# Optimization experiments

Measured on AMD Instinct MI355X. Metric: run time of the kernel, lower is better.

## Reference

```python
import jax, jax.numpy as jnp
import numpy as np

WINDOW_SIZE = 11
SIGMA = 1.5

def _gauss1d(n, sigma):
    xs = (jnp.arange(n) - n // 2).astype(jnp.float32)
    g = jnp.exp(-(xs ** 2) / (2.0 * sigma ** 2))
    return g / g.sum()

def _blur3d(v, g):
    # Separable 3D Gaussian blur == dense outer-product 3D window used by the
    # original (the torch window is an exact outer product of 1D gaussians).
    C = v.shape[1]
    k = g.shape[0]
    p = k // 2
    for ax in range(3):
        kshape = [1, 1, 1]
        kshape[ax] = k
        w = jnp.broadcast_to(g.reshape(tuple(kshape))[None, None], (C, 1) + tuple(kshape))
        pad = [(0, 0), (0, 0), (0, 0)]
        pad[ax] = (p, p)
        v = jax.lax.conv_general_dilated(
            v, w, window_strides=(1, 1, 1), padding=pad,
            dimension_numbers=('NCDHW', 'OIDHW', 'NCDHW'),
            feature_group_count=C)
    return v

def _ssim(a, b, size_average=True):
    g = _gauss1d(WINDOW_SIZE, SIGMA)
    mu1 = _blur3d(a, g)
    mu2 = _blur3d(b, g)
    mu1_sq = mu1 * mu1
    mu2_sq = mu2 * mu2
    sigma1_sq = _blur3d(a * a, g) - mu1_sq
    sigma2_sq = _blur3d(b * b, g) - mu2_sq
    sigma12 = _blur3d(a * b, g) - mu1 * mu2
    C1, C2 = 0.01 ** 2, 0.03 ** 2
    ssim_map = ((2.0 * mu1 * mu2 + C1) * (2.0 * sigma12 + C2)) / \
               ((mu1_sq + mu2_sq + C1) * (sigma1_sq + sigma2_sq + C2))
    if size_average:
        return ssim_map.mean()
    return ssim_map.mean(axis=(1, 2, 3))

def reference(x, y, z, modality):
    # modality: 0 -> 'PET' (compare x vs z), 1 -> 'CT' (compare x vs y)
    if modality == 0:
        s = _ssim(x, z)
    else:
        s = _ssim(x, y)
    return (1.0 - s) ** 2

def setup_inputs() -> dict:
    key = jax.random.key(0)
    k1, k2, k3 = jax.random.split(key, 3)
    shape = (2, 1, 192, 192, 192)
    x = jax.random.uniform(k1, shape, dtype=jnp.float32)
    y = jax.random.uniform(k2, shape, dtype=jnp.float32)
    z = jax.random.uniform(k3, shape, dtype=jnp.float32)
    return {"x": x, "y": y, "z": z, "modality": 0}
```

## Files before the change

kernel.cpp:

```cpp
#include <hip/hip_runtime.h>
#include <math.h>

#define NW 192
#define NH 192
#define ND 192
#define NB 2
#define SLICE (NH * NW)
#define SLICEB (SLICE * 4)
#define VOLB (ND * SLICEB)
#define VOLF ((double)(NB) * ND * NH * NW)
#define NF4 (NW / 4)

#define TH 16
#define TW 16
#define HALO 5
#define LHH (TH + 2 * HALO)
#define DC 48
#define NITER ((DC + 2 * HALO) / 2)
#define TPS (LHH * (TW / 4))
#define NTASK (2 * TPS)
#define FSTR (LHH * TW)
#define WTILES (NW / TW)
#define HTILES (NH / TH)
#define DCHUNKS (ND / DC)
#define TILES (WTILES * HTILES)
#define NBLOCKS (TILES * DCHUNKS * NB)
#define NXCD 8
#define CPX (NBLOCKS / NXCD)

typedef float f32x4 __attribute__((ext_vector_type(4)));
typedef int   i32x4 __attribute__((ext_vector_type(4)));

__device__ f32x4 llvm_buf_load_x4(i32x4 rsrc, int voffset, int soffset, int aux)
    __asm("llvm.amdgcn.raw.buffer.load.v4f32");

__device__ __forceinline__ i32x4 make_srd(const void* p, unsigned bytes) {
    union { i32x4 v; struct { const void* p; unsigned nrec; unsigned fl; } s; } u;
    u.s.p = p;
    u.s.nrec = bytes;
    u.s.fl = 0x00020000;
    return u.v;
}

__device__ unsigned g_done = 0;

struct GaussK { float g[11]; };

template <bool FAST>
__device__ __forceinline__ float ssim_tile(
    const float* __restrict__ xb, const float* __restrict__ bb,
    int h0, int w0, int d0, const GaussK& G, float* tw, int tid)
{
    const int tx = tid & 15, ty = tid >> 4;
    const bool is_strip = (tid < NTASK);
    const int s_of = tid / TPS;
    const int r_of = (tid % TPS) >> 2;
    const int c_of = tid & 3;
    const int gh = h0 - HALO + r_of;
    const int f4base = (w0 >> 2) + c_of - 2;
    float* twp = tw + s_of * 5 * FSTR + r_of * TW + 4 * c_of;
    const float* trd = tw + ty * TW + tx;

    const i32x4 rsA = make_srd(xb, VOLB);
    const i32x4 rsB = make_srd(bb, VOLB);
    const int wb = gh * (NW * 4) + f4base * 16;
    const int offbase = (d0 - HALO + s_of) * SLICEB + wb;
    const bool row_ok = is_strip && ((unsigned)gh < (unsigned)NH);
    const long rowb4 = (long)gh * NF4;
    const f32x4* xb4 = (const f32x4*)xb;
    const f32x4* bb4 = (const f32x4*)bb;

    float acc0[12], acc1[12], acc2[12], acc3[12], acc4[12];
#pragma unroll
    for (int j = 0; j < 12; ++j) { acc0[j]=0.f; acc1[j]=0.f; acc2[j]=0.f; acc3[j]=0.f; acc4[j]=0.f; }
    float vA[5], vB[5];
    float sum = 0.f;

    auto d_round = [&](int J) {
#pragma unroll
        for (int j = 0; j < 11; ++j) {
            const float g = G.g[j];
            acc0[j] += g * vA[0]; acc1[j] += g * vA[1]; acc2[j] += g * vA[2];
            acc3[j] += g * vA[3]; acc4[j] += g * vA[4];
        }
#pragma unroll
        for (int j = 1; j < 12; ++j) {
            const float g = G.g[j - 1];
            acc0[j] += g * vB[0]; acc1[j] += g * vB[1]; acc2[j] += g * vB[2];
            acc3[j] += g * vB[3]; acc4[j] += g * vB[4];
        }
        if (J >= 5) {
#pragma unroll
            for (int e = 0; e < 2; ++e) {
                const float mu1 = acc0[e], mu2 = acc1[e];
                const float mu1sq = mu1 * mu1, mu2sq = mu2 * mu2, mu12 = mu1 * mu2;
                const float s1 = acc2[e] - mu1sq;
                const float s2 = acc3[e] - mu2sq;
                const float s12 = acc4[e] - mu12;
                const float C1 = 1e-4f, C2 = 9e-4f;
                const float num = (2.f * mu12 + C1) * (2.f * s12 + C2);
                const float den = (mu1sq + mu2sq + C1) * (s1 + s2 + C2);
                sum += num * __builtin_amdgcn_rcpf(den);
            }
        }
#pragma unroll
        for (int j = 0; j < 10; ++j) {
            acc0[j] = acc0[j+2]; acc1[j] = acc1[j+2]; acc2[j] = acc2[j+2];
            acc3[j] = acc3[j+2]; acc4[j] = acc4[j+2];
        }
        acc0[10]=0.f; acc1[10]=0.f; acc2[10]=0.f; acc3[10]=0.f; acc4[10]=0.f;
        acc0[11]=0.f; acc1[11]=0.f; acc2[11]=0.f; acc3[11]=0.f; acc4[11]=0.f;
    };

#pragma unroll 1
    for (int it = 0; it < NITER; ++it) {
        f32x4 pa[5], pb[5];
        if (is_strip) {
            if (FAST) {
                const int off = offbase + it * (2 * SLICEB);
#pragma unroll
                for (int k = 0; k < 5; ++k) {
                    pa[k] = llvm_buf_load_x4(rsA, off + 16 * k, 0, 0);
                    pb[k] = llvm_buf_load_x4(rsB, off + 16 * k, 0, 0);
                }
            } else {
                const int dd = d0 - HALO + 2 * it + s_of;
                const bool okd = row_ok && ((unsigned)dd < (unsigned)ND);
                const long sb4 = (long)dd * (SLICE / 4) + rowb4;
#pragma unroll
                for (int k = 0; k < 5; ++k) {
                    const int f4 = f4base + k;
                    const bool ok = okd && ((unsigned)f4 < (unsigned)NF4);
                    f32x4 va = {0.f, 0.f, 0.f, 0.f}, vb = {0.f, 0.f, 0.f, 0.f};
                    if (ok) { va = xb4[sb4 + f4]; vb = bb4[sb4 + f4]; }
                    pa[k] = va; pb[k] = vb;
                }
            }
        }

        if (it > 0) d_round(it - 1);

        if (is_strip) {
            float A[4]={0,0,0,0}, Bv[4]={0,0,0,0}, A2[4]={0,0,0,0},
                  B2[4]={0,0,0,0}, AB[4]={0,0,0,0};
#pragma unroll
            for (int k = 0; k < 5; ++k) {
#pragma unroll
                for (int e = 0; e < 4; ++e) {
                    const int idx = 4 * k + e;
                    if (idx < 3 || idx > 16) continue;
                    const float a = pa[k][e];
                    const float b = pb[k][e];
                    const float a2 = a * a, b2 = b * b, ab = a * b;
#pragma unroll
                    for (int j = 0; j < 4; ++j) {
                        const int u = idx - 3 - j;
                        if (u < 0 || u > 10) continue;
                        const float g = G.g[u];
                        A[j]  += g * a;  Bv[j] += g * b;
                        A2[j] += g * a2; B2[j] += g * b2; AB[j] += g * ab;
                    }
                }
            }
            ((float4*)(twp + 0 * FSTR))[0] = make_float4(A[0], A[1], A[2], A[3]);
            ((float4*)(twp + 1 * FSTR))[0] = make_float4(Bv[0], Bv[1], Bv[2], Bv[3]);
            ((float4*)(twp + 2 * FSTR))[0] = make_float4(A2[0], A2[1], A2[2], A2[3]);
            ((float4*)(twp + 3 * FSTR))[0] = make_float4(B2[0], B2[1], B2[2], B2[3]);
            ((float4*)(twp + 4 * FSTR))[0] = make_float4(AB[0], AB[1], AB[2], AB[3]);
        }
        __syncthreads();

#pragma unroll
        for (int s2 = 0; s2 < 2; ++s2) {
#pragma unroll
            for (int f = 0; f < 5; ++f) {
                const float* p = trd + (s2 * 5 + f) * FSTR;
                float a = 0.f;
#pragma unroll
                for (int v = 0; v < 11; ++v) a += G.g[v] * p[v * TW];
                if (s2 == 0) vA[f] = a; else vB[f] = a;
            }
        }
        __syncthreads();
    }
    d_round(NITER - 1);
    return sum;
}

__global__ __launch_bounds__(256)
void k_ssim_fused(const float* __restrict__ x, const float* __restrict__ y,
                  const float* __restrict__ z, const int* __restrict__ mod,
                  float* __restrict__ out, GaussK G)
{
    __shared__ float tw[2 * 5 * FSTR];
    __shared__ float wred[4];

    const int tid = threadIdx.x;

    const unsigned lin = blockIdx.x +
        (unsigned)gridDim.x * (blockIdx.y + (unsigned)gridDim.y * blockIdx.z);
    const unsigned work = (lin & (NXCD - 1)) * CPX + (lin >> 3);
    const unsigned tile = work % TILES;
    const unsigned rest = work / TILES;
    const int wt = tile % WTILES, ht = tile / WTILES;
    const int d0 = (int)(rest % DCHUNKS) * DC;
    const int n  = (int)(rest / DCHUNKS);
    const int h0 = ht * TH, w0 = wt * TW;

    const float* bsel = (*mod == 0) ? z : y;
    const float* xb = x + (size_t)n * ND * SLICE;
    const float* bb = bsel + (size_t)n * ND * SLICE;

    const bool interior = (ht > 0) & (ht < HTILES - 1) & (wt > 0) & (wt < WTILES - 1);
    float sum;
    if (interior) sum = ssim_tile<true >(xb, bb, h0, w0, d0, G, tw, tid);
    else          sum = ssim_tile<false>(xb, bb, h0, w0, d0, G, tw, tid);

    float v = sum;
#pragma unroll
    for (int off = 32; off > 0; off >>= 1) v += __shfl_down(v, off, 64);
    if ((tid & 63) == 0) wred[tid >> 6] = v;
    __syncthreads();
    if (tid == 0) {
        const float bsum = wred[0] + wred[1] + wred[2] + wred[3];
        atomicAdd(out, bsum);
        __threadfence();
        unsigned old = atomicAdd(&g_done, 1u);
        if (old == (unsigned)(NBLOCKS - 1)) {
            float total = atomicAdd(out, 0.f);
            double m = 1.0 - (double)total / VOLF;
            out[0] = (float)(m * m);
            __threadfence();
            atomicExch(&g_done, 0u);
        }
    }
}

extern "C" void kernel_launch(void* const* d_in, const int* in_sizes, int n_in,
                              void* d_out, int out_size, void* d_ws, size_t ws_size,
                              hipStream_t stream) {
    const float* x = (const float*)d_in[0];
    const float* y = (const float*)d_in[1];
    const float* z = (const float*)d_in[2];
    const int* modality = (const int*)d_in[3];
    float* out = (float*)d_out;

    GaussK G;
    {
        double raw[11], s = 0.0;
        for (int i = 0; i < 11; ++i) {
            double dx = (double)(i - 5);
            raw[i] = exp(-(dx * dx) / (2.0 * 1.5 * 1.5));
            s += raw[i];
        }
        for (int i = 0; i < 11; ++i) G.g[i] = (float)(raw[i] / s);
    }

    dim3 grid(WTILES * HTILES, ND / DC, NB);
    k_ssim_fused<<<grid, 256, 0, stream>>>(x, y, z, modality, out, G);
}
```

Baseline: 325.9 us.

## Restructure H-pass so 160 threads each compute a full sliding column

Before, each of the 256 threads applied the 11-tap H-direction blur independently for its own output, so every input was loaded 11 times per field. Now 160 threads each own one (field, column) pair, stream the 26 halo rows once and accumulate all 16 outputs in registers. The results are written to a new padded shared buffer that the D-pass threads then read. This cuts LDS reads and redundant FMAs in exchange for extra shared memory, an extra LDS write/read round trip, and 96 threads sitting idle during this phase.

New measurement: 313.2 us. 1.04x faster.

```diff
diff --git a/kernel.cpp b/kernel.cpp
--- a/kernel.cpp
+++ b/kernel.cpp
@@ -19,7 +19,6 @@
 #define NITER ((DC + 2 * HALO) / 2)
 #define TPS (LHH * (TW / 4))
 #define NTASK (2 * TPS)
-#define FSTR (LHH * TW)
 #define WTILES (NW / TW)
 #define HTILES (NH / TH)
 #define DCHUNKS (ND / DC)
@@ -28,6 +27,12 @@
 #define NXCD 8
 #define CPX (NBLOCKS / NXCD)
 
+#define FPAD 424
+#define TWSZ (10 * FPAD)
+#define HB_CSTR 20
+#define HB_PSTR 320
+#define HBSZ (10 * HB_PSTR)
+
 typedef float f32x4 __attribute__((ext_vector_type(4)));
 typedef int   i32x4 __attribute__((ext_vector_type(4)));
 
@@ -49,7 +54,7 @@
 template <bool FAST>
 __device__ __forceinline__ float ssim_tile(
     const float* __restrict__ xb, const float* __restrict__ bb,
-    int h0, int w0, int d0, const GaussK& G, float* tw, int tid)
+    int h0, int w0, int d0, const GaussK& G, float* tw, float* hbuf, int tid)
 {
     const int tx = tid & 15, ty = tid >> 4;
     const bool is_strip = (tid < NTASK);
@@ -58,8 +63,12 @@
     const int c_of = tid & 3;
     const int gh = h0 - HALO + r_of;
     const int f4base = (w0 >> 2) + c_of - 2;
-    float* twp = tw + s_of * 5 * FSTR + r_of * TW + 4 * c_of;
-    const float* trd = tw + ty * TW + tx;
+    float* twp = tw + s_of * 5 * FPAD + r_of * TW + 4 * c_of;
+
+    const bool is_col = (tid < 160);
+    const float* cbase = tw + (tid >> 4) * FPAD + (tid & 15);
+    float* hwr = hbuf + (tid >> 4) * HB_PSTR + (tid & 15) * HB_CSTR;
+    const float* hrd = hbuf + tx * HB_CSTR + ty;
 
     const i32x4 rsA = make_srd(xb, VOLB);
     const i32x4 rsB = make_srd(bb, VOLB);
@@ -73,10 +82,9 @@
     float acc0[12], acc1[12], acc2[12], acc3[12], acc4[12];
 #pragma unroll
     for (int j = 0; j < 12; ++j) { acc0[j]=0.f; acc1[j]=0.f; acc2[j]=0.f; acc3[j]=0.f; acc4[j]=0.f; }
-    float vA[5], vB[5];
     float sum = 0.f;
 
-    auto d_round = [&](int J) {
+    auto d_round = [&](const float* vA, const float* vB, int J) {
 #pragma unroll
         for (int j = 0; j < 11; ++j) {
             const float g = G.g[j];
@@ -138,7 +146,15 @@
             }
         }
 
-        if (it > 0) d_round(it - 1);
+        if (it > 0) {
+            float vA[5], vB[5];
+#pragma unroll
+            for (int f = 0; f < 5; ++f) {
+                vA[f] = hrd[f * HB_PSTR];
+                vB[f] = hrd[(5 + f) * HB_PSTR];
+            }
+            d_round(vA, vB, it - 1);
+        }
 
         if (is_strip) {
             float A[4]={0,0,0,0}, Bv[4]={0,0,0,0}, A2[4]={0,0,0,0},
@@ -162,28 +178,43 @@
                     }
                 }
             }
-            ((float4*)(twp + 0 * FSTR))[0] = make_float4(A[0], A[1], A[2], A[3]);
-            ((float4*)(twp + 1 * FSTR))[0] = make_float4(Bv[0], Bv[1], Bv[2], Bv[3]);
-            ((float4*)(twp + 2 * FSTR))[0] = make_float4(A2[0], A2[1], A2[2], A2[3]);
-            ((float4*)(twp + 3 * FSTR))[0] = make_float4(B2[0], B2[1], B2[2], B2[3]);
-            ((float4*)(twp + 4 * FSTR))[0] = make_float4(AB[0], AB[1], AB[2], AB[3]);
+            ((float4*)(twp + 0 * FPAD))[0] = make_float4(A[0], A[1], A[2], A[3]);
+            ((float4*)(twp + 1 * FPAD))[0] = make_float4(Bv[0], Bv[1], Bv[2], Bv[3]);
+            ((float4*)(twp + 2 * FPAD))[0] = make_float4(A2[0], A2[1], A2[2], A2[3]);
+            ((float4*)(twp + 3 * FPAD))[0] = make_float4(B2[0], B2[1], B2[2], B2[3]);
+            ((float4*)(twp + 4 * FPAD))[0] = make_float4(AB[0], AB[1], AB[2], AB[3]);
         }
         __syncthreads();
 
-#pragma unroll
-        for (int s2 = 0; s2 < 2; ++s2) {
-#pragma unroll
-            for (int f = 0; f < 5; ++f) {
-                const float* p = trd + (s2 * 5 + f) * FSTR;
-                float a = 0.f;
-#pragma unroll
-                for (int v = 0; v < 11; ++v) a += G.g[v] * p[v * TW];
-                if (s2 == 0) vA[f] = a; else vB[f] = a;
-            }
+        if (is_col) {
+            float o[16];
+#pragma unroll
+            for (int r = 0; r < 16; ++r) o[r] = 0.f;
+#pragma unroll
+            for (int r = 0; r < 26; ++r) {
+                const float w = cbase[r * TW];
+                const int jlo = (r - 10 < 0) ? 0 : r - 10;
+                const int jhi = (r < 15) ? r : 15;
+#pragma unroll
+                for (int j = jlo; j <= jhi; ++j) o[j] += G.g[r - j] * w;
+            }
+            ((float4*)(hwr + 0))[0]  = make_float4(o[0],  o[1],  o[2],  o[3]);
+            ((float4*)(hwr + 4))[0]  = make_float4(o[4],  o[5],  o[6],  o[7]);
+            ((float4*)(hwr + 8))[0]  = make_float4(o[8],  o[9],  o[10], o[11]);
+            ((float4*)(hwr + 12))[0] = make_float4(o[12], o[13], o[14], o[15]);
         }
         __syncthreads();
     }
-    d_round(NITER - 1);
+
+    {
+        float vA[5], vB[5];
+#pragma unroll
+        for (int f = 0; f < 5; ++f) {
+            vA[f] = hrd[f * HB_PSTR];
+            vB[f] = hrd[(5 + f) * HB_PSTR];
+        }
+        d_round(vA, vB, NITER - 1);
+    }
     return sum;
 }
 
@@ -192,7 +223,8 @@
                   const float* __restrict__ z, const int* __restrict__ mod,
                   float* __restrict__ out, GaussK G)
 {
-    __shared__ float tw[2 * 5 * FSTR];
+    __shared__ float tw[TWSZ];
+    __shared__ float hbuf[HBSZ];
     __shared__ float wred[4];
 
     const int tid = threadIdx.x;
@@ -213,8 +245,8 @@
 
     const bool interior = (ht > 0) & (ht < HTILES - 1) & (wt > 0) & (wt < WTILES - 1);
     float sum;
-    if (interior) sum = ssim_tile<true >(xb, bb, h0, w0, d0, G, tw, tid);
-    else          sum = ssim_tile<false>(xb, bb, h0, w0, d0, G, tw, tid);
+    if (interior) sum = ssim_tile<true >(xb, bb, h0, w0, d0, G, tw, hbuf, tid);
+    else          sum = ssim_tile<false>(xb, bb, h0, w0, d0, G, tw, hbuf, tid);
 
     float v = sum;
 #pragma unroll
```
